# Optimization experiments

Measured on AMD Instinct MI355X. Metric: run time of the kernel, lower is better.

The kernel has to match this reference:

```python
import jax, jax.numpy as jnp
import numpy as np

B, N, C = 2, 2048, 1024
H, HD = 16, 64
PX, PY, PS = 24, 24, 16  # S2RoPE head_dim split (px+py+ps == head_dim)


def rotate_half(t):
    t1, t2 = jnp.split(t, 2, axis=-1)
    return jnp.concatenate([-t2, t1], axis=-1)


def apply_phase_rope(t, phase):
    # t: [B, N, H, d_seg] (d_seg even), phase: [B, N, d_seg//2] angles in radians
    ang = jnp.concatenate([phase, phase], axis=-1)[:, :, None, :]  # [B,N,1,d_seg]
    return t * jnp.cos(ang) + rotate_half(t) * jnp.sin(ang)


def s2rope(t, phase_x, phase_y, phase_sph):
    # spherical RoPE: rotate three disjoint segments of head_dim by the
    # per-token x / y / spherical phases
    tx, ty, ts = t[..., :PX], t[..., PX:PX + PY], t[..., PX + PY:]
    return jnp.concatenate([
        apply_phase_rope(tx, phase_x),
        apply_phase_rope(ty, phase_y),
        apply_phase_rope(ts, phase_sph),
    ], axis=-1)


def setup_inputs() -> dict:
    key = jax.random.key(0)
    ks = jax.random.split(key, 9)
    two_pi = 6.2831853
    return {
        "x": jax.random.normal(ks[0], (B, N, C), dtype=jnp.float32),
        "phase_x": jax.random.uniform(ks[1], (B, N, PX // 2), dtype=jnp.float32) * two_pi,
        "phase_y": jax.random.uniform(ks[2], (B, N, PY // 2), dtype=jnp.float32) * two_pi,
        "phase_sph": jax.random.uniform(ks[3], (B, N, PS // 2), dtype=jnp.float32) * two_pi,
        "rope_mask": jax.random.randint(ks[4], (B, N), 0, 2).astype(bool),
        "Wqkv": jax.random.normal(ks[5], (C, 3 * C), dtype=jnp.float32) * (C ** -0.5),
        "bqkv": jax.random.normal(ks[6], (3 * C,), dtype=jnp.float32) * 0.02,
        "Wproj": jax.random.normal(ks[7], (C, C), dtype=jnp.float32) * (C ** -0.5),
        "bproj": jax.random.normal(ks[8], (C,), dtype=jnp.float32) * 0.02,
    }


def reference(x, phase_x, phase_y, phase_sph, rope_mask, Wqkv, bqkv, Wproj, bproj):
    # qkv projection -> [B, N, 3, H, HD]
    qkv = (x @ Wqkv + bqkv).reshape(B, N, 3, H, HD)
    q, k, v = qkv[:, :, 0], qkv[:, :, 1], qkv[:, :, 2]  # each [B, N, H, HD]

    # template path: S2RoPE with rope_mask selecting which tokens are rotated
    q_rope = s2rope(q, phase_x, phase_y, phase_sph)
    k_rope = s2rope(k, phase_x, phase_y, phase_sph)
    m = rope_mask[:, :, None, None]  # [B, N, 1, 1]
    q = jnp.where(m, q_rope, q)
    k = jnp.where(m, k_rope, k)

    scale = HD ** -0.5
    # [B, H, N, N] scores, softmax over keys, then weighted sum of values
    attn = jax.nn.softmax(jnp.einsum('bnhd,bmhd->bhnm', q, k) * scale, axis=-1)
    out = jnp.einsum('bhnm,bmhd->bnhd', attn, v).reshape(B, N, C)
    return out @ Wproj + bproj
```

## Files before the change

kernel.cpp:

```cpp
#include <hip/hip_runtime.h>
#include <hip/hip_fp16.h>

typedef _Float16 f16;
typedef unsigned int u32;
typedef _Float16 f16x4 __attribute__((ext_vector_type(4)));
typedef _Float16 f16x8 __attribute__((ext_vector_type(8)));
typedef float f32x4 __attribute__((ext_vector_type(4)));
typedef float f32x16 __attribute__((ext_vector_type(16)));

#define B_  2
#define N_  2048
#define C_  1024
#define H_  16
#define HD_ 64

__device__ __forceinline__ void gload_lds16(const void* g, void* l) {
  __builtin_amdgcn_global_load_lds((const __attribute__((address_space(1))) u32*)g,
                                   (__attribute__((address_space(3))) u32*)l,
                                   16, 0, 0);
}

__device__ __forceinline__ u32 pack_f16(float a, float b) {
  auto h2 = __builtin_amdgcn_cvt_pkrtz(a, b);
  return __builtin_bit_cast(u32, h2);
}

__device__ __forceinline__ float max3f(float a, float b, float c) {
  return fmaxf(fmaxf(a, b), c);
}

__global__ void detect_mask(const u32* __restrict__ m, int* __restrict__ flag) {
  __shared__ int bad;
  if (threadIdx.x == 0) bad = 0;
  __syncthreads();
  int v = 0;
  for (int i = threadIdx.x; i < 1024; i += 256) {
    u32 w = m[i];
    if (w != 0u && w != 1u && w != 0x3F800000u) v = 1;
  }
  if (v) atomicOr(&bad, 1);
  __syncthreads();
  if (threadIdx.x == 0) *flag = bad;
}

__global__ __launch_bounds__(256) void phase_tab(const float* __restrict__ px,
                                                 const float* __restrict__ py,
                                                 const float* __restrict__ psp,
                                                 const void* __restrict__ maskPtr,
                                                 const int* __restrict__ maskFlag,
                                                 float* __restrict__ cs_tab,
                                                 float* __restrict__ sn_tab) {
  const int idx = blockIdx.x * 256 + threadIdx.x;
  const int j = idx & 31, tn = idx >> 5;
  const int byteMode = *maskFlag;
  const bool doRope = byteMode ? (((const unsigned char*)maskPtr)[tn] != 0)
                               : (((const u32*)maskPtr)[tn] != 0u);
  float c = 1.f, s = 0.f;
  if (doRope) {
    float ph;
    if (j < 12)      ph = px[tn * 12 + j];
    else if (j < 24) ph = py[tn * 12 + (j - 12)];
    else             ph = psp[tn * 8 + (j - 24)];
    c = __cosf(ph);
    s = __sinf(ph);
  }
  cs_tab[idx] = c;
  sn_tab[idx] = s;
}

__global__ __launch_bounds__(256) void cvt_x(const float* __restrict__ in,
                                             f16* __restrict__ out, int n8) {
  const int i = blockIdx.x * 256 + threadIdx.x;
  if (i >= n8) return;
  const float4 a = ((const float4*)in)[i * 2];
  const float4 b = ((const float4*)in)[i * 2 + 1];
  f16x8 o = {(f16)a.x, (f16)a.y, (f16)a.z, (f16)a.w,
             (f16)b.x, (f16)b.y, (f16)b.z, (f16)b.w};
  ((f16x8*)out)[i] = o;
}

__global__ __launch_bounds__(256) void transpose_cvt(const float* __restrict__ W,
                                                     f16* __restrict__ Wt,
                                                     int R, int Ccols) {
  __shared__ __align__(16) f16 tile[32][34];
  const int c0 = blockIdx.x * 32, r0 = blockIdx.y * 32;
  const int tx = threadIdx.x, ty = threadIdx.y;
#pragma unroll
  for (int k = 0; k < 4; ++k)
    tile[ty + 8 * k][tx] = (f16)W[(size_t)(r0 + ty + 8 * k) * Ccols + c0 + tx];
  __syncthreads();
#pragma unroll
  for (int k = 0; k < 4; ++k)
    Wt[(size_t)(c0 + ty + 8 * k) * R + r0 + tx] = tile[tx][ty + 8 * k];
}

template <bool OUT_F32>
__global__ __launch_bounds__(256) void gemm_bt(const f16* __restrict__ A,
                                               const f16* __restrict__ Bt,
                                               const float* __restrict__ bias,
                                               void* __restrict__ Cout,
                                               int M, int N, int K) {
  __shared__ __align__(16) f16 As[128 * 64];
  __shared__ __align__(16) f16 Bs[128 * 64];
  const int tid = threadIdx.x;
  const int lane = tid & 63;
  const int wv = tid >> 6;
  const int wm = wv >> 1, wn = wv & 1;
  const int nTN = N >> 7;
  int bid = blockIdx.x;
  const int cpx = gridDim.x >> 3;
  bid = (bid & 7) * cpx + (bid >> 3);
  const int tM = bid / nTN, tN = bid % nTN;
  const int rowBase = tM << 7, colBase = tN << 7;
  const int cl = lane & 15, cg = lane >> 4;

  f32x4 acc[4][4];
#pragma unroll
  for (int i = 0; i < 4; ++i)
#pragma unroll
    for (int j = 0; j < 4; ++j) acc[i][j] = (f32x4){0.f, 0.f, 0.f, 0.f};

  const int sR = tid >> 3, sC = tid & 7;

  for (int k0 = 0; k0 < K; k0 += 64) {
#pragma unroll
    for (int is = 0; is < 4; ++is) {
      const int r = is * 32 + sR;
      const int sc = sC ^ (r & 7);
      gload_lds16(A + (size_t)(rowBase + r) * K + k0 + sc * 8, As + is * 2048 + tid * 8);
    }
#pragma unroll
    for (int is = 0; is < 4; ++is) {
      const int r = is * 32 + sR;
      const int sc = sC ^ (r & 7);
      gload_lds16(Bt + (size_t)(colBase + r) * K + k0 + sc * 8, Bs + is * 2048 + tid * 8);
    }
    asm volatile("s_waitcnt vmcnt(0)" ::: "memory");
    __syncthreads();

#pragma unroll
    for (int ks = 0; ks < 2; ++ks) {
      f16x8 af[4], bf[4];
#pragma unroll
      for (int m = 0; m < 4; ++m) {
        const int row = wm * 64 + m * 16 + cl;
        const int ck = (ks * 4 + cg) ^ (row & 7);
        af[m] = *(const f16x8*)(As + row * 64 + ck * 8);
      }
#pragma unroll
      for (int n = 0; n < 4; ++n) {
        const int row = wn * 64 + n * 16 + cl;
        const int ck = (ks * 4 + cg) ^ (row & 7);
        bf[n] = *(const f16x8*)(Bs + row * 64 + ck * 8);
      }
#pragma unroll
      for (int m = 0; m < 4; ++m)
#pragma unroll
        for (int n = 0; n < 4; ++n)
          acc[m][n] = __builtin_amdgcn_mfma_f32_16x16x32_f16(af[m], bf[n], acc[m][n], 0, 0, 0);
    }
    __syncthreads();
  }

#pragma unroll
  for (int m = 0; m < 4; ++m) {
#pragma unroll
    for (int n = 0; n < 4; ++n) {
      const int gr0 = rowBase + wm * 64 + m * 16 + cg * 4;
      const int gc = colBase + wn * 64 + n * 16 + cl;
      const float bz = bias[gc];
#pragma unroll
      for (int reg = 0; reg < 4; ++reg) {
        const float v = acc[m][n][reg] + bz;
        if (OUT_F32)
          ((float*)Cout)[(size_t)(gr0 + reg) * N + gc] = v;
        else
          ((f16*)Cout)[(size_t)(gr0 + reg) * N + gc] = (f16)v;
      }
    }
  }
}

__global__ __launch_bounds__(256) void rope_split(const f16* __restrict__ qkv,
                                                  const float* __restrict__ cs_tab,
                                                  const float* __restrict__ sn_tab,
                                                  f16* __restrict__ Qh,
                                                  f16* __restrict__ Kh,
                                                  f16* __restrict__ Vt) {
  __shared__ float cs[64][32], sn[64][32];
  __shared__ __align__(16) f16 vtile[64][72];
  const int tid = threadIdx.x;
  const int blk = blockIdx.x;
  const int hg = blk & 3;
  const int nt = (blk >> 2) & 31;
  const int b = blk >> 7;
  const int n0 = nt * 64;

  for (int i = tid; i < 64 * 32; i += 256) {
    const int tk = i >> 5, j = i & 31;
    const size_t gi = ((size_t)b * N_ + n0 + tk) * 32 + j;
    cs[tk][j] = cs_tab[gi];
    sn[tk][j] = sn_tab[gi];
  }
  __syncthreads();

  const int tk = tid >> 2, hl = tid & 3;
  const int h = hg * 4 + hl;
  const int n = n0 + tk;
  const size_t inRow = ((size_t)b * N_ + n) * 3072 + (size_t)h * 64;
  const size_t outRow = (((size_t)(b * H_ + h)) * N_ + n) * 64;

#pragma unroll
  for (int sec = 0; sec < 2; ++sec) {
    const f16* src = qkv + inRow + sec * 1024;
    float t[64];
#pragma unroll
    for (int c = 0; c < 8; ++c) {
      f16x8 v = *(const f16x8*)(src + c * 8);
#pragma unroll
      for (int j = 0; j < 8; ++j) t[c * 8 + j] = (float)v[j];
    }
    __align__(16) f16 o[64];
#pragma unroll
    for (int d = 0; d < 64; ++d) {
      int j;
      float rot;
      if (d < 24) {
        j = (d < 12) ? d : d - 12;
        rot = (d < 12) ? -t[d + 12] : t[d - 12];
      } else if (d < 48) {
        const int dd = d - 24;
        j = 12 + ((dd < 12) ? dd : dd - 12);
        rot = (dd < 12) ? -t[d + 12] : t[d - 12];
      } else {
        const int dd = d - 48;
        j = 24 + ((dd < 8) ? dd : dd - 8);
        rot = (dd < 8) ? -t[d + 8] : t[d - 8];
      }
      o[d] = (f16)(t[d] * cs[tk][j] + rot * sn[tk][j]);
    }
    f16* dst = (sec == 0 ? Qh : Kh) + outRow;
#pragma unroll
    for (int c = 0; c < 8; ++c) *(f16x8*)(dst + c * 8) = *(const f16x8*)(o + c * 8);
  }

  for (int hl2 = 0; hl2 < 4; ++hl2) {
    const int h2 = hg * 4 + hl2;
    __syncthreads();
    {
      const int tk2 = tid >> 2, c2 = tid & 3;
      const size_t srow = ((size_t)b * N_ + n0 + tk2) * 3072 + 2048 + (size_t)h2 * 64 + c2 * 16;
      *(f16x8*)(&vtile[tk2][c2 * 16]) = *(const f16x8*)(qkv + srow);
      *(f16x8*)(&vtile[tk2][c2 * 16 + 8]) = *(const f16x8*)(qkv + srow + 8);
    }
    __syncthreads();
    {
      const int d = tid >> 2, seg = tid & 3;
      __align__(16) f16 tmp[16];
#pragma unroll
      for (int i = 0; i < 16; ++i) tmp[i] = vtile[seg * 16 + i][d];
      const size_t drow = (((size_t)(b * H_ + h2)) * 64 + d) * N_ + n0 + seg * 16;
      *(f16x8*)(Vt + drow) = *(const f16x8*)(tmp);
      *(f16x8*)(Vt + drow + 8) = *(const f16x8*)(tmp + 8);
    }
  }
}

__global__ __launch_bounds__(256) void attn2(const f16* __restrict__ Qh,
                                             const f16* __restrict__ Kh,
                                             const f16* __restrict__ Vt,
                                             f16* __restrict__ Y) {
  __shared__ __align__(16) f16 lds[2][2][4096];
  const int tid = threadIdx.x, lane = tid & 63, w = tid >> 6;
  int bid = blockIdx.x;
  bid = (bid & 7) * 64 + (bid >> 3);
  const int bh = bid >> 4, qb = bid & 15;
  const int b = bh >> 4, h = bh & 15;
  const f16* Qb = Qh + (size_t)bh * N_ * 64;
  const f16* Kb = Kh + (size_t)bh * N_ * 64;
  const f16* Vb = Vt + (size_t)bh * 64 * N_;
  const int ql = lane & 31, hi = lane >> 5;

  f16x8 qf[4];
  {
    const int qrow = qb * 128 + w * 32 + ql;
    const f16 scl = (f16)0.125f;
#pragma unroll
    for (int ks = 0; ks < 4; ++ks) {
      f16x8 v = *(const f16x8*)(Qb + (size_t)qrow * 64 + ks * 16 + hi * 8);
#pragma unroll
      for (int j = 0; j < 8; ++j) v[j] *= scl;
      qf[ks] = v;
    }
  }

  f32x16 Of[2];
#pragma unroll
  for (int d = 0; d < 2; ++d)
#pragma unroll
    for (int r = 0; r < 16; ++r) Of[d][r] = 0.f;
  float m_run = -1e30f, l_run = 0.f;

  const int sr = tid >> 3, sc = tid & 7;
#define STAGE(t, bb)                                                                     \
  {                                                                                      \
    _Pragma("unroll") for (int i = 0; i < 2; ++i) {                                      \
      const int row = i * 32 + sr;                                                       \
      const int g = sc ^ (row & 7);                                                      \
      gload_lds16(Kb + (size_t)((t) * 64 + row) * 64 + g * 8,                            \
                  &lds[bb][0][i * 2048 + tid * 8]);                                      \
    }                                                                                    \
    _Pragma("unroll") for (int i = 0; i < 2; ++i) {                                      \
      const int row = i * 32 + sr;                                                       \
      const int g = sc ^ (row & 7);                                                      \
      gload_lds16(Vb + (size_t)row * N_ + (t) * 64 + g * 8,                              \
                  &lds[bb][1][i * 2048 + tid * 8]);                                      \
    }                                                                                    \
  }

#define SOFTMAX_CHUNK(sa)                                                                \
  {                                                                                      \
    float t0 = max3f(sa[0], sa[1], sa[2]);                                               \
    float t1 = max3f(sa[3], sa[4], sa[5]);                                               \
    float t2 = max3f(sa[6], sa[7], sa[8]);                                               \
    float t3 = max3f(sa[9], sa[10], sa[11]);                                             \
    float t4 = max3f(sa[12], sa[13], sa[14]);                                            \
    float pmax = max3f(max3f(t0, t1, t2), max3f(t3, t4, sa[15]), -1e30f);                \
    pmax = fmaxf(pmax, __shfl_xor(pmax, 32));                                            \
    if (__any(pmax > m_run + 8.0f)) {                                                    \
      const float mnew = fmaxf(m_run, pmax);                                             \
      const float corr = __expf(m_run - mnew);                                           \
      l_run *= corr;                                                                     \
      _Pragma("unroll") for (int d = 0; d < 2; ++d)                                      \
        _Pragma("unroll") for (int r = 0; r < 16; ++r) Of[d][r] *= corr;                 \
      m_run = mnew;                                                                      \
    }                                                                                    \
    _Pragma("unroll") for (int r = 0; r < 16; ++r) sa[r] = __expf(sa[r] - m_run);        \
    float s0 = ((sa[0] + sa[1]) + (sa[2] + sa[3])) + ((sa[4] + sa[5]) + (sa[6] + sa[7]));\
    float s1 = ((sa[8] + sa[9]) + (sa[10] + sa[11])) +                                   \
               ((sa[12] + sa[13]) + (sa[14] + sa[15]));                                  \
    float ssum = s0 + s1;                                                                \
    ssum += __shfl_xor(ssum, 32);                                                        \
    l_run += ssum;                                                                       \
  }

#define PV_CHUNK(sa, s)                                                                  \
  {                                                                                      \
    u32 pw[8];                                                                           \
    _Pragma("unroll") for (int tt = 0; tt < 8; ++tt)                                     \
      pw[tt] = pack_f16(sa[2 * tt], sa[2 * tt + 1]);                                     \
    _Pragma("unroll") for (int kk = 0; kk < 2; ++kk) {                                   \
      u32 a0 = pw[4 * kk], a1 = pw[4 * kk + 1];                                          \
      u32 b0 = pw[4 * kk + 2], b1 = pw[4 * kk + 3];                                      \
      asm volatile("v_permlane32_swap_b32 %0, %1" : "+v"(a0), "+v"(b0));                 \
      asm volatile("v_permlane32_swap_b32 %0, %1" : "+v"(a1), "+v"(b1));                 \
      union { u32 u[4]; f16x8 v; } pf;                                                   \
      pf.u[0] = a0; pf.u[1] = a1; pf.u[2] = b0; pf.u[3] = b1;                            \
      __builtin_amdgcn_s_setprio(1);                                                     \
      _Pragma("unroll") for (int df = 0; df < 2; ++df) {                                 \
        const int d = df * 32 + ql;                                                      \
        f16x8 vf = *(const f16x8*)(Vs + d * 64 + (((s) * 4 + kk * 2 + hi) ^ (d & 7)) * 8);\
        Of[df] = __builtin_amdgcn_mfma_f32_32x32x16_f16(vf, pf.v, Of[df], 0, 0, 0);      \
      }                                                                                  \
      __builtin_amdgcn_s_setprio(0);                                                     \
    }                                                                                    \
  }

  STAGE(0, 0);
  asm volatile("s_waitcnt vmcnt(0)" ::: "memory");
  __syncthreads();

  int cur = 0;
  for (int t = 0; t < N_ / 64; ++t) {
    if (t < N_ / 64 - 1) STAGE(t + 1, cur ^ 1);
    const f16* Ks = &lds[cur][0][0];
    const f16* Vs = &lds[cur][1][0];

    f32x16 sa0, sa1;
#pragma unroll
    for (int r = 0; r < 16; ++r) { sa0[r] = 0.f; sa1[r] = 0.f; }
    const int krow0 = ql, krow1 = 32 + ql;
    __builtin_amdgcn_s_setprio(1);
#pragma unroll
    for (int ks = 0; ks < 4; ++ks) {
      f16x8 kf = *(const f16x8*)(Ks + krow0 * 64 + ((ks * 2 + hi) ^ (krow0 & 7)) * 8);
      sa0 = __builtin_amdgcn_mfma_f32_32x32x16_f16(kf, qf[ks], sa0, 0, 0, 0);
    }
#pragma unroll
    for (int ks = 0; ks < 4; ++ks) {
      f16x8 kf = *(const f16x8*)(Ks + krow1 * 64 + ((ks * 2 + hi) ^ (krow1 & 7)) * 8);
      sa1 = __builtin_amdgcn_mfma_f32_32x32x16_f16(kf, qf[ks], sa1, 0, 0, 0);
    }
    __builtin_amdgcn_s_setprio(0);

    SOFTMAX_CHUNK(sa0);
    PV_CHUNK(sa0, 0);
    SOFTMAX_CHUNK(sa1);
    PV_CHUNK(sa1, 1);

    asm volatile("s_waitcnt vmcnt(0)" ::: "memory");
    __syncthreads();
    cur ^= 1;
  }

  const float inv = 1.0f / l_run;
  f16* Ow = &lds[0][0][0] + w * (32 * 72);
#pragma unroll
  for (int df = 0; df < 2; ++df)
#pragma unroll
    for (int g = 0; g < 4; ++g) {
      f16x4 ov;
#pragma unroll
      for (int e = 0; e < 4; ++e) ov[e] = (f16)(Of[df][g * 4 + e] * inv);
      *(f16x4*)(Ow + ql * 72 + df * 32 + g * 8 + hi * 4) = ov;
    }
  __syncthreads();
  const int rr = lane >> 1, half = lane & 1;
  const f16* srcp = Ow + rr * 72 + half * 32;
  const int nglob = qb * 128 + w * 32 + rr;
  f16* dst = Y + ((size_t)b * N_ + nglob) * C_ + h * 64 + half * 32;
#pragma unroll
  for (int c2 = 0; c2 < 4; ++c2)
    *(f16x8*)(dst + c2 * 8) = *(const f16x8*)(srcp + c2 * 8);
}

extern "C" void kernel_launch(void* const* d_in, const int* in_sizes, int n_in,
                              void* d_out, int out_size, void* d_ws, size_t ws_size,
                              hipStream_t stream) {
  const float* x = (const float*)d_in[0];
  const float* px = (const float*)d_in[1];
  const float* py = (const float*)d_in[2];
  const float* psp = (const float*)d_in[3];
  const void* mask = (const void*)d_in[4];
  const float* Wqkv = (const float*)d_in[5];
  const float* bqkv = (const float*)d_in[6];
  const float* Wproj = (const float*)d_in[7];
  const float* bproj = (const float*)d_in[8];
  float* out = (float*)d_out;
  char* ws = (char*)d_ws;

  f16* xh     = (f16*)(ws + 0);
  f16* Wqkvt  = (f16*)(ws + 8388608);
  f16* Wprojt = (f16*)(ws + 14680064);
  f16* qkvh   = (f16*)(ws + 16777216);
  f16* Qh     = (f16*)(ws + 41943040);
  f16* Kh     = (f16*)(ws + 50331648);
  f16* Vt     = (f16*)(ws + 58720256);
  f16* Yh     = (f16*)(ws + 67108864);
  int* mflag  = (int*)(ws + 75497472);
  float* cs_tab = (float*)(ws + 67108864);
  float* sn_tab = (float*)(ws + 67108864 + 524288);

  detect_mask<<<1, 256, 0, stream>>>((const u32*)mask, mflag);
  cvt_x<<<2048, 256, 0, stream>>>(x, xh, (B_ * N_ * C_) / 8);
  phase_tab<<<512, 256, 0, stream>>>(px, py, psp, mask, mflag, cs_tab, sn_tab);
  transpose_cvt<<<dim3(96, 32), dim3(32, 8), 0, stream>>>(Wqkv, Wqkvt, C_, 3 * C_);
  transpose_cvt<<<dim3(32, 32), dim3(32, 8), 0, stream>>>(Wproj, Wprojt, C_, C_);
  gemm_bt<false><<<(4096 / 128) * (3072 / 128), 256, 0, stream>>>(
      xh, Wqkvt, bqkv, (void*)qkvh, 4096, 3072, 1024);
  rope_split<<<256, 256, 0, stream>>>(qkvh, cs_tab, sn_tab, Qh, Kh, Vt);
  attn2<<<512, 256, 0, stream>>>(Qh, Kh, Vt, Yh);
  gemm_bt<true><<<(4096 / 128) * (1024 / 128), 256, 0, stream>>>(
      Yh, Wprojt, bproj, (void*)out, 4096, 1024, 1024);
}
```

Baseline: 161.3 us.

## Triple-buffer K/V tiles in attention and defer row-sum cross-lane reduction

Switches the attention kernel's LDS staging from double to triple buffering, prefetching two tiles ahead. Each iteration now waits with partial vmcnt instead of draining all loads and uses a raw s_barrier, so global loads overlap compute more deeply. The per-chunk shuffle for the softmax denominator moves out of the loop to a single cross-lane reduction at the end. The cost is more LDS (48KB per block), which may lower occupancy, plus more delicate waitcnt accounting.

```diff
diff --git a/kernel.cpp b/kernel.cpp
--- a/kernel.cpp
+++ b/kernel.cpp
@@ -270,7 +270,7 @@
                                              const f16* __restrict__ Kh,
                                              const f16* __restrict__ Vt,
                                              f16* __restrict__ Y) {
-  __shared__ __align__(16) f16 lds[2][2][4096];
+  __shared__ __align__(16) f16 lds_flat[3 * 8192];
   const int tid = threadIdx.x, lane = tid & 63, w = tid >> 6;
   int bid = blockIdx.x;
   bid = (bid & 7) * 64 + (bid >> 3);
@@ -302,19 +302,18 @@
   float m_run = -1e30f, l_run = 0.f;
 
   const int sr = tid >> 3, sc = tid & 7;
-#define STAGE(t, bb)                                                                     \
+#define STAGE(t, bp)                                                                     \
   {                                                                                      \
     _Pragma("unroll") for (int i = 0; i < 2; ++i) {                                      \
       const int row = i * 32 + sr;                                                       \
       const int g = sc ^ (row & 7);                                                      \
-      gload_lds16(Kb + (size_t)((t) * 64 + row) * 64 + g * 8,                            \
-                  &lds[bb][0][i * 2048 + tid * 8]);                                      \
+      gload_lds16(Kb + (size_t)((t) * 64 + row) * 64 + g * 8, (bp) + i * 2048 + tid * 8);\
     }                                                                                    \
     _Pragma("unroll") for (int i = 0; i < 2; ++i) {                                      \
       const int row = i * 32 + sr;                                                       \
       const int g = sc ^ (row & 7);                                                      \
       gload_lds16(Vb + (size_t)row * N_ + (t) * 64 + g * 8,                              \
-                  &lds[bb][1][i * 2048 + tid * 8]);                                      \
+                  (bp) + 4096 + i * 2048 + tid * 8);                                     \
     }                                                                                    \
   }
 
@@ -339,9 +338,7 @@
     float s0 = ((sa[0] + sa[1]) + (sa[2] + sa[3])) + ((sa[4] + sa[5]) + (sa[6] + sa[7]));\
     float s1 = ((sa[8] + sa[9]) + (sa[10] + sa[11])) +                                   \
                ((sa[12] + sa[13]) + (sa[14] + sa[15]));                                  \
-    float ssum = s0 + s1;                                                                \
-    ssum += __shfl_xor(ssum, 32);                                                        \
-    l_run += ssum;                                                                       \
+    l_run += s0 + s1;                                                                    \
   }
 
 #define PV_CHUNK(sa, s)                                                                  \
@@ -366,15 +363,18 @@
     }                                                                                    \
   }
 
-  STAGE(0, 0);
-  asm volatile("s_waitcnt vmcnt(0)" ::: "memory");
-  __syncthreads();
-
-  int cur = 0;
+  f16* const base = &lds_flat[0];
+  STAGE(0, base);
+  STAGE(1, base + 8192);
+  asm volatile("s_waitcnt vmcnt(4)" ::: "memory");
+  __builtin_amdgcn_s_barrier();
+
+  f16* curp = base;
+  f16* stagep = base + 16384;
   for (int t = 0; t < N_ / 64; ++t) {
-    if (t < N_ / 64 - 1) STAGE(t + 1, cur ^ 1);
-    const f16* Ks = &lds[cur][0][0];
-    const f16* Vs = &lds[cur][1][0];
+    if (t < N_ / 64 - 2) STAGE(t + 2, stagep);
+    const f16* Ks = curp;
+    const f16* Vs = curp + 4096;
 
     f32x16 sa0, sa1;
 #pragma unroll
@@ -398,13 +398,20 @@
     SOFTMAX_CHUNK(sa1);
     PV_CHUNK(sa1, 1);
 
-    asm volatile("s_waitcnt vmcnt(0)" ::: "memory");
-    __syncthreads();
-    cur ^= 1;
-  }
-
-  const float inv = 1.0f / l_run;
-  f16* Ow = &lds[0][0][0] + w * (32 * 72);
+    if (t < N_ / 64 - 2)
+      asm volatile("s_waitcnt vmcnt(4) lgkmcnt(0)" ::: "memory");
+    else if (t < N_ / 64 - 1)
+      asm volatile("s_waitcnt vmcnt(0) lgkmcnt(0)" ::: "memory");
+    else
+      asm volatile("s_waitcnt lgkmcnt(0)" ::: "memory");
+    __builtin_amdgcn_s_barrier();
+    curp = (curp == base + 16384) ? base : curp + 8192;
+    stagep = (stagep == base + 16384) ? base : stagep + 8192;
+  }
+
+  const float l_tot = l_run + __shfl_xor(l_run, 32);
+  const float inv = 1.0f / l_tot;
+  f16* Ow = base + w * (32 * 72);
 #pragma unroll
   for (int df = 0; df < 2; ++df)
 #pragma unroll
```

Measured after the change: 160.2 us. No clear change (-0.7%).
